# Performance work log

Hardware: AMD Instinct MI355X
Metric: run time of the kernel (lower is better)

## Reference

```python
import jax, jax.numpy as jnp
import numpy as np

N, D = 2048, 1024
OUT = 65536
S = 16384  # number of LSH-selected neurons


def setup_inputs() -> dict:
    key = jax.random.key(0)
    k1, k2, k3, k4 = jax.random.split(key, 4)
    x = jax.random.normal(k1, (N, D), dtype=jnp.float32)
    # original init: uniform(-1, 1) weights, zero bias; use randn-scale weights per spec
    weight = jax.random.normal(k2, (OUT, D), dtype=jnp.float32)
    bias = jax.random.normal(k3, (OUT,), dtype=jnp.float32)
    sample_ids = jax.random.randint(k4, (S,), 0, OUT, dtype=jnp.int64)
    return {"x": x, "weight": weight, "bias": bias, "sample_ids": sample_ids}


def reference(x, weight, bias, sample_ids):
    # Gather selected neuron rows (F.embedding equivalent)
    sample_weights = weight[sample_ids]          # [S, D]
    sample_bias = bias[sample_ids]               # [S]
    # x @ W_sel.T + b_sel  -> [N, S]
    sample_logits = jnp.einsum('nd,sd->ns', x, sample_weights) + sample_bias
    return sample_logits
```

## Files before the change

kernel.cpp:

```cpp
#include <hip/hip_runtime.h>
#include <stdint.h>


typedef __bf16 bf16x8 __attribute__((ext_vector_type(8)));
typedef float f32x4 __attribute__((ext_vector_type(4)));

#define BM 128
#define BN 128
#define BK 64

__device__ __forceinline__ ushort f2bf(float f) {
  union { float f; uint32_t u; } c; c.f = f;
  uint32_t u = c.u;
  return (ushort)((u + 0x7FFFu + ((u >> 16) & 1u)) >> 16);
}

__global__ __launch_bounds__(256) void prep_kernel(
    const float* __restrict__ x, const float* __restrict__ W,
    const float* __restrict__ bias, const int* __restrict__ ids,
    ushort* __restrict__ Wg, ushort* __restrict__ xb,
    float* __restrict__ biasg, int D, int S) {
  const int t = threadIdx.x;
  const int gblocks = S >> 3;
  if ((int)blockIdx.x < gblocks) {
    const int s0 = blockIdx.x << 3;
    if (t < 8) biasg[s0 + t] = bias[ids[s0 + t]];
#pragma unroll
    for (int r = 0; r < 8; ++r) {
      const int s = s0 + r;
      const int id = ids[s];
      float4 v = ((const float4*)(W + (size_t)id * D))[t];
      ushort4 o;
      o.x = f2bf(v.x); o.y = f2bf(v.y); o.z = f2bf(v.z); o.w = f2bf(v.w);
      ((ushort4*)(Wg + (size_t)s * D))[t] = o;
    }
  } else {
    const int i = (blockIdx.x - gblocks) * 256 + t;
    float4 v = ((const float4*)x)[i];
    ushort4 o;
    o.x = f2bf(v.x); o.y = f2bf(v.y); o.z = f2bf(v.z); o.w = f2bf(v.w);
    ((ushort4*)xb)[i] = o;
  }
}

__device__ __forceinline__ void load_lds16(const void* g, void* l) {
  __builtin_amdgcn_global_load_lds(
      (const __attribute__((address_space(1))) void*)g,
      (__attribute__((address_space(3))) void*)l, 16, 0, 0);
}

__device__ __forceinline__ const ushort* frag_ptr(const ushort* base, int row,
                                                  int c) {
  return base + row * BK + (((c ^ (row & 7)) << 3));
}

__global__ __launch_bounds__(256) void gemm_bt_bias(
    const ushort* __restrict__ A, const ushort* __restrict__ B,
    const float* __restrict__ biasg, float* __restrict__ C,
    int M, int S, int K) {
  __shared__ __align__(16) ushort As[BM * BK];
  __shared__ __align__(16) ushort Bs[BN * BK];

  const int tid  = threadIdx.x;
  const int lane = tid & 63;
  const int wave = tid >> 6;
  const int bn = blockIdx.x;
  const int bm = blockIdx.y;

  const int wm = (wave >> 1) * 64;
  const int wn = (wave & 1) * 64;
  const int quad = lane >> 4;
  const int l16  = lane & 15;

  const int srow = tid >> 3;
  const int scol = (((tid & 7) ^ (srow & 7)) << 3);
  const ushort* Ag = A + (size_t)(bm * BM + srow) * K + scol;
  const ushort* Bg = B + (size_t)(bn * BN + srow) * K + scol;
  ushort* Asl = As + tid * 8;
  ushort* Bsl = Bs + tid * 8;

  f32x4 acc[4][4] = {};

  for (int kt = 0; kt < K; kt += BK) {
#pragma unroll
    for (int i = 0; i < 4; ++i) {
      load_lds16(Ag + (size_t)(i * 32) * K, Asl + i * 32 * BK);
      load_lds16(Bg + (size_t)(i * 32) * K, Bsl + i * 32 * BK);
    }
    Ag += BK; Bg += BK;
    __syncthreads();

#pragma unroll
    for (int ks = 0; ks < BK; ks += 32) {
      const int c0 = (ks >> 3) + quad;
      bf16x8 af[4], bq[4];
#pragma unroll
      for (int i = 0; i < 4; ++i)
        af[i] = *(const bf16x8*)frag_ptr(As, wm + i * 16 + l16, c0);
#pragma unroll
      for (int j = 0; j < 4; ++j)
        bq[j] = *(const bf16x8*)frag_ptr(Bs, wn + j * 16 + l16, c0);
#pragma unroll
      for (int i = 0; i < 4; ++i)
#pragma unroll
        for (int j = 0; j < 4; ++j)
          acc[i][j] = __builtin_amdgcn_mfma_f32_16x16x32_bf16(
              af[i], bq[j], acc[i][j], 0, 0, 0);
    }
    __syncthreads();
  }

  const int row0 = bm * BM + wm + quad * 4;
  const int col0 = bn * BN + wn + l16;
#pragma unroll
  for (int j = 0; j < 4; ++j) {
    const int col = col0 + j * 16;
    const float bv = biasg[col];
#pragma unroll
    for (int i = 0; i < 4; ++i) {
#pragma unroll
      for (int r = 0; r < 4; ++r) {
        C[(size_t)(row0 + i * 16 + r) * S + col] = acc[i][j][r] + bv;
      }
    }
  }
}

extern "C" void kernel_launch(void* const* d_in, const int* in_sizes, int n_in,
                              void* d_out, int out_size, void* d_ws, size_t ws_size,
                              hipStream_t stream) {
  const float* x    = (const float*)d_in[0];
  const float* W    = (const float*)d_in[1];
  const float* bias = (const float*)d_in[2];
  const int*   ids  = (const int*)d_in[3];
  float* out = (float*)d_out;

  const int OUTN = in_sizes[2];
  const int S    = in_sizes[3];
  const int D    = in_sizes[1] / OUTN;
  const int N    = in_sizes[0] / D;

  ushort* Wg = (ushort*)d_ws;
  ushort* xb = (ushort*)((char*)d_ws + (size_t)S * D * sizeof(ushort));
  float* biasg = (float*)((char*)d_ws + (size_t)S * D * sizeof(ushort)
                          + (size_t)N * D * sizeof(ushort));

  const int gather_blocks = S / 8;
  const int conv_blocks = (N * D) / 1024;
  prep_kernel<<<gather_blocks + conv_blocks, 256, 0, stream>>>(
      x, W, bias, ids, Wg, xb, biasg, D, S);

  dim3 grid(S / BN, N / BM);
  gemm_bt_bias<<<grid, 256, 0, stream>>>(xb, Wg, biasg, out, N, S, D);
}
```

Measured before the change: 430.8 us.

## Enlarge GEMM tiles to 256x256 with double-buffered LDS and interleaved prefetch

Raises the block tile to 256x256 and runs 512 threads (8 waves, each owning 128x64). Shared memory is double-buffered so the next K-tile's global-to-LDS loads are issued while MFMAs run on the current tile. Fragment loads are split into quadrants interleaved with MFMA groups, and MFMA priority is raised with setprio. The aim is more data reuse per loaded byte and latency hiding, in exchange for heavier register and LDS use (128KB LDS per block) and fewer blocks in the grid.

```diff
diff --git a/kernel.cpp b/kernel.cpp
--- a/kernel.cpp
+++ b/kernel.cpp
@@ -5,8 +5,8 @@
 typedef __bf16 bf16x8 __attribute__((ext_vector_type(8)));
 typedef float f32x4 __attribute__((ext_vector_type(4)));
 
-#define BM 128
-#define BN 128
+#define BM 256
+#define BN 256
 #define BK 64
 
 __device__ __forceinline__ ushort f2bf(float f) {
@@ -49,78 +49,122 @@
       (__attribute__((address_space(3))) void*)l, 16, 0, 0);
 }
 
-__device__ __forceinline__ const ushort* frag_ptr(const ushort* base, int row,
-                                                  int c) {
-  return base + row * BK + (((c ^ (row & 7)) << 3));
-}
-
-__global__ __launch_bounds__(256) void gemm_bt_bias(
+__global__ __launch_bounds__(512, 2) void gemm_bt_bias(
     const ushort* __restrict__ A, const ushort* __restrict__ B,
     const float* __restrict__ biasg, float* __restrict__ C,
     int M, int S, int K) {
-  __shared__ __align__(16) ushort As[BM * BK];
-  __shared__ __align__(16) ushort Bs[BN * BK];
+  __shared__ __align__(16) ushort As[2 * BM * BK];
+  __shared__ __align__(16) ushort Bs[2 * BN * BK];
 
   const int tid  = threadIdx.x;
   const int lane = tid & 63;
   const int wave = tid >> 6;
+  const int wm = (wave >> 2) * 128;
+  const int wn = (wave & 3) * 64;
+  const int quad = lane >> 4;
+  const int l16  = lane & 15;
   const int bn = blockIdx.x;
   const int bm = blockIdx.y;
 
-  const int wm = (wave >> 1) * 64;
-  const int wn = (wave & 1) * 64;
-  const int quad = lane >> 4;
-  const int l16  = lane & 15;
-
   const int srow = tid >> 3;
   const int scol = (((tid & 7) ^ (srow & 7)) << 3);
-  const ushort* Ag = A + (size_t)(bm * BM + srow) * K + scol;
-  const ushort* Bg = B + (size_t)(bn * BN + srow) * K + scol;
-  ushort* Asl = As + tid * 8;
-  ushort* Bsl = Bs + tid * 8;
+  const ushort* Asrc = A + (size_t)(bm * BM + srow) * K + scol;
+  const ushort* Bsrc = B + (size_t)(bn * BN + srow) * K + scol;
 
-  f32x4 acc[4][4] = {};
+  const int pc0 = ((quad ^ (l16 & 7)) << 3);
+  const int pc1 = (((4 + quad) ^ (l16 & 7)) << 3);
 
-  for (int kt = 0; kt < K; kt += BK) {
+  f32x4 acc[8][4] = {};
+
+  auto stage_tile = [&](const ushort* src, ushort* dst, int kt) {
+#pragma unroll
+    for (int j = 0; j < 4; ++j)
+      load_lds16(src + (size_t)(j * 64) * K + kt, dst + (j * 512 + tid) * 8);
+  };
+
+  auto load_af = [&](const ushort* Acur, int ih, bf16x8 (&af)[4][2]) {
 #pragma unroll
     for (int i = 0; i < 4; ++i) {
-      load_lds16(Ag + (size_t)(i * 32) * K, Asl + i * 32 * BK);
-      load_lds16(Bg + (size_t)(i * 32) * K, Bsl + i * 32 * BK);
+      const int ro = (wm + (ih * 4 + i) * 16 + l16) * BK;
+      af[i][0] = *(const bf16x8*)(Acur + ro + pc0);
+      af[i][1] = *(const bf16x8*)(Acur + ro + pc1);
     }
-    Ag += BK; Bg += BK;
-    __syncthreads();
-
+  };
+  auto load_bq = [&](const ushort* Bcur, int jh, bf16x8 (&bq)[2][2]) {
 #pragma unroll
-    for (int ks = 0; ks < BK; ks += 32) {
-      const int c0 = (ks >> 3) + quad;
-      bf16x8 af[4], bq[4];
+    for (int j = 0; j < 2; ++j) {
+      const int ro = (wn + (jh * 2 + j) * 16 + l16) * BK;
+      bq[j][0] = *(const bf16x8*)(Bcur + ro + pc0);
+      bq[j][1] = *(const bf16x8*)(Bcur + ro + pc1);
+    }
+  };
+  auto mma_q = [&](bf16x8 (&af)[4][2], bf16x8 (&bq)[2][2], int ih, int jh) {
+    __builtin_amdgcn_s_setprio(1);
 #pragma unroll
-      for (int i = 0; i < 4; ++i)
-        af[i] = *(const bf16x8*)frag_ptr(As, wm + i * 16 + l16, c0);
-#pragma unroll
-      for (int j = 0; j < 4; ++j)
-        bq[j] = *(const bf16x8*)frag_ptr(Bs, wn + j * 16 + l16, c0);
+    for (int ks = 0; ks < 2; ++ks)
 #pragma unroll
       for (int i = 0; i < 4; ++i)
 #pragma unroll
-        for (int j = 0; j < 4; ++j)
-          acc[i][j] = __builtin_amdgcn_mfma_f32_16x16x32_bf16(
-              af[i], bq[j], acc[i][j], 0, 0, 0);
+        for (int j = 0; j < 2; ++j)
+          acc[ih * 4 + i][jh * 2 + j] =
+              __builtin_amdgcn_mfma_f32_16x16x32_bf16(
+                  af[i][ks], bq[j][ks], acc[ih * 4 + i][jh * 2 + j], 0, 0, 0);
+    __builtin_amdgcn_s_setprio(0);
+  };
+
+  stage_tile(Asrc, (ushort*)As, 0);
+  stage_tile(Bsrc, (ushort*)Bs, 0);
+
+  const int NT = K / BK;
+  for (int t = 0; t < NT; ++t) {
+    const int cur = t & 1;
+    const ushort* Acur = (const ushort*)As + cur * (BM * BK);
+    const ushort* Bcur = (const ushort*)Bs + cur * (BN * BK);
+    ushort* Anx = (ushort*)As + (cur ^ 1) * (BM * BK);
+    ushort* Bnx = (ushort*)Bs + (cur ^ 1) * (BN * BK);
+    const int kn = (t + 1) * BK;
+
+    if (t + 1 < NT) {
+      stage_tile(Asrc, Anx, kn);
+      asm volatile("s_waitcnt vmcnt(4)" ::: "memory");
+    } else {
+      asm volatile("s_waitcnt vmcnt(0)" ::: "memory");
     }
-    __syncthreads();
+    __builtin_amdgcn_sched_barrier(0);
+    __builtin_amdgcn_s_barrier();
+    __builtin_amdgcn_sched_barrier(0);
+
+    bf16x8 af[4][2], bq0[2][2], bq1[2][2];
+    load_af(Acur, 0, af);
+    load_bq(Bcur, 0, bq0);
+    mma_q(af, bq0, 0, 0);
+
+    if (t + 1 < NT) stage_tile(Bsrc, Bnx, kn);
+    load_bq(Bcur, 1, bq1);
+    mma_q(af, bq1, 0, 1);
+
+    load_af(Acur, 1, af);
+    mma_q(af, bq1, 1, 1);
+
+    load_bq(Bcur, 0, bq0);
+    mma_q(af, bq0, 1, 0);
+
+    __builtin_amdgcn_sched_barrier(0);
+    __builtin_amdgcn_s_barrier();
+    __builtin_amdgcn_sched_barrier(0);
   }
 
   const int row0 = bm * BM + wm + quad * 4;
   const int col0 = bn * BN + wn + l16;
 #pragma unroll
-  for (int j = 0; j < 4; ++j) {
-    const int col = col0 + j * 16;
+  for (int jf = 0; jf < 4; ++jf) {
+    const int col = col0 + jf * 16;
     const float bv = biasg[col];
 #pragma unroll
-    for (int i = 0; i < 4; ++i) {
+    for (int i = 0; i < 8; ++i) {
 #pragma unroll
       for (int r = 0; r < 4; ++r) {
-        C[(size_t)(row0 + i * 16 + r) * S + col] = acc[i][j][r] + bv;
+        C[(size_t)(row0 + i * 16 + r) * S + col] = acc[i][jf][r] + bv;
       }
     }
   }
@@ -151,5 +195,5 @@
       x, W, bias, ids, Wg, xb, biasg, D, S);
 
   dim3 grid(S / BN, N / BM);
-  gemm_bt_bias<<<grid, 256, 0, stream>>>(xb, Wg, biasg, out, N, S, D);
+  gemm_bt_bias<<<grid, 512, 0, stream>>>(xb, Wg, biasg, out, N, S, D);
 }
```

Measured after the change: 450.4 us. +4.6%, slower.
